# Optimization experiments

Measured on AMD Instinct MI355X. Metric: run time of the kernel, lower is better.

## Reference

```python
import jax, jax.numpy as jnp
import numpy as np


def _encode(tab, idx):
    # tab: [F, V, D]; idx: [..., F] int -> sum_f tab[f, idx[..., f]] -> [..., D]
    g = jax.vmap(lambda t, i: t[i], in_axes=(0, -1), out_axes=0)(tab, idx)
    return g.sum(0)


def _diffuse(fea, ei, w, order):
    # fea: [N, D]; ei: [2, E]; w: [E] learned edge weights
    N = fea.shape[0]
    r, c = ei[0], ei[1]
    adj = jnp.zeros((N, N), fea.dtype).at[r, c].set(w).at[c, r].set(w)
    adj = adj + jnp.eye(N, dtype=fea.dtype)
    r_col_inv = adj.sum(1) ** -0.5  # from degree over axis 1
    r_row_inv = adj.sum(0) ** -0.5  # from degree over axis 0
    A = r_row_inv[:, None] * adj * r_col_inv[None, :]
    x = fea
    y = fea
    for _ in range(order):
        x = jax.lax.stop_gradient(A @ x)
        y = y + x
    return jax.lax.stop_gradient(y / (order + 1.0))


def setup_inputs():
    B, N, E, EMB, L, FA, FB, V = 512, 128, 512, 300, 5, 9, 3, 64
    k = jax.random.split(jax.random.key(0), 12)
    s = 0.02
    return {
        "order": 3,
        "x_atom": jax.random.randint(k[0], (B, N, FA), 0, V),
        "edge_index": jax.random.randint(k[1], (B, 2, E), 0, N),
        "edge_attr": jax.random.randint(k[2], (B, E, FB), 0, V),
        "atom_tab": jax.random.normal(k[3], (FA, V, EMB)) * s,
        "bond_tab_root": jax.random.normal(k[4], (FB, V, EMB)) * s,
        "edge_lin_w": jax.random.normal(k[5], (EMB,)) * s,
        "edge_lin_b": jnp.zeros(()),
        "bond_tabs": jax.random.normal(k[6], (L, FB, V, EMB)) * s,
        "eps": jnp.zeros((L,)),
        "w1": jax.random.normal(k[7], (L, EMB, 2 * EMB)) * s,
        "b1": jnp.zeros((L, 2 * EMB)),
        "bn1_g": jnp.ones((L, 2 * EMB)),
        "bn1_b": jnp.zeros((L, 2 * EMB)),
        "w2": jax.random.normal(k[8], (L, 2 * EMB, EMB)) * s,
        "b2": jnp.zeros((L, EMB)),
        "bn_g": jnp.ones((L, EMB)),
        "bn_b": jnp.zeros((L, EMB)),
    }


def reference(order, x_atom, edge_index, edge_attr, atom_tab, bond_tab_root,
              edge_lin_w, edge_lin_b, bond_tabs, eps, w1, b1, bn1_g, bn1_b,
              w2, b2, bn_g, bn_b):
    B, N = x_atom.shape[:2]
    E = edge_index.shape[-1]
    L = w1.shape[0]
    DROP = 0.2  # node-feature drop rate (eval-mode scaling)

    # --- per-graph dense-adjacency diffusion (vmapped over graphs) ---
    fea = _encode(atom_tab, x_atom) * (1.0 - DROP)                 # [B, N, D]
    e_emb = _encode(bond_tab_root, edge_attr)                      # [B, E, D]
    ew = jax.nn.sigmoid(e_emb @ edge_lin_w + edge_lin_b)           # [B, E]
    h = jax.vmap(_diffuse, in_axes=(0, 0, 0, None))(fea, edge_index, ew, order)
    h = h.reshape(B * N, -1)                                       # [B*N, D]

    # --- globally-batched GIN message passing ---
    off = (jnp.arange(B) * N)[:, None]
    src = (edge_index[:, 0, :] + off).reshape(-1)                  # [B*E]
    dst = (edge_index[:, 1, :] + off).reshape(-1)
    ea_flat = edge_attr.reshape(B * E, -1)

    for l in range(L):
        ee = _encode(bond_tabs[l], ea_flat)                        # [B*E, D]
        msg = jax.nn.relu(h[src] + ee)
        agg = jax.ops.segment_sum(msg, dst, num_segments=B * N)
        z = (1.0 + eps[l]) * h + agg
        z = z @ w1[l] + b1[l]
        z = bn1_g[l] * z + bn1_b[l]   # eval-mode BN (running mean 0, var 1)
        z = jax.nn.relu(z)
        z = z @ w2[l] + b2[l]
        z = bn_g[l] * z + bn_b[l]     # outer eval-mode BN
        if l < L - 1:
            z = jax.nn.relu(z)
        h = z
    return h
```

## Files before the change

### kernel.cpp

```cpp
#include <hip/hip_runtime.h>

#define NGRAPH 512
#define NNODE  128
#define NEDGE  512
#define EMB    300
#define NLAYER 5
#define FA     9
#define FB     3
#define VV     64
#define KPAD   136

typedef __bf16 bf16x8 __attribute__((ext_vector_type(8)));
typedef __bf16 bf16x4 __attribute__((ext_vector_type(4)));
typedef float  f32x4  __attribute__((ext_vector_type(4)));

__device__ __forceinline__ void gload_lds16(const void* gptr, void* lptr) {
    __builtin_amdgcn_global_load_lds(
        (const __attribute__((address_space(1))) void*)gptr,
        (__attribute__((address_space(3))) void*)lptr, 16, 0, 0);
}

__global__ __launch_bounds__(256)
void prep_w_kernel(const float* __restrict__ w1, const float* __restrict__ w2,
                   __bf16* __restrict__ w1t, __bf16* __restrict__ w2t)
{
    const int i = blockIdx.x * 256 + threadIdx.x;
    const int T1 = NLAYER * 640 * 320;
    const int T2 = NLAYER * 320 * 640;
    if (i < T1) {
        const int l = i / (640 * 320);
        const int r = i - l * 640 * 320;
        const int n = r / 320, k = r - n * 320;
        float v = (n < 600 && k < 300) ? w1[((size_t)l * 300 + k) * 600 + n] : 0.f;
        w1t[i] = (__bf16)v;
    } else if (i < T1 + T2) {
        const int j = i - T1;
        const int l = j / (320 * 640);
        const int r = j - l * 320 * 640;
        const int n = r / 640, k = r - n * 640;
        float v = (n < 300 && k < 600) ? w2[((size_t)l * 600 + k) * 300 + n] : 0.f;
        w2t[j] = (__bf16)v;
    }
}

__global__ __launch_bounds__(512)
void adj_kernel(const int* __restrict__ edge_index,
                const int* __restrict__ edge_attr,
                const float* __restrict__ bond_tab_root,
                const float* __restrict__ edge_lin_w,
                const float* __restrict__ edge_lin_b,
                __bf16* __restrict__ Ahi_g, __bf16* __restrict__ Alo_g)
{
    __shared__ float A[128 * 129];
    __shared__ float ew_s[NEDGE];
    __shared__ int   es[NEDGE];
    __shared__ float rinv[128];
    __shared__ float cinv[128];

    const int tid = threadIdx.x;
    const int g   = blockIdx.x;
    int* Ai = (int*)A;

    for (int e = tid; e < NEDGE; e += 512) {
        int r = edge_index[(g * 2 + 0) * NEDGE + e];
        int c = edge_index[(g * 2 + 1) * NEDGE + e];
        es[e] = r | (c << 8);
    }
    for (int i = tid; i < 128 * 129; i += 512) Ai[i] = -1;
    __syncthreads();

    {
        const int wave = tid >> 6, lane = tid & 63;
        const float elb = edge_lin_b[0];
        for (int e = wave * 64; e < wave * 64 + 64; ++e) {
            const int base = (g * NEDGE + e) * 3;
            const int a0 = edge_attr[base + 0];
            const int a1 = edge_attr[base + 1];
            const int a2 = edge_attr[base + 2];
            const float* t0 = bond_tab_root + (0 * VV + a0) * EMB;
            const float* t1 = bond_tab_root + (1 * VV + a1) * EMB;
            const float* t2 = bond_tab_root + (2 * VV + a2) * EMB;
            float acc = 0.f;
            for (int d = lane; d < EMB; d += 64)
                acc += (t0[d] + t1[d] + t2[d]) * edge_lin_w[d];
            #pragma unroll
            for (int off = 32; off > 0; off >>= 1) acc += __shfl_xor(acc, off, 64);
            if (lane == 0) ew_s[e] = 1.f / (1.f + expf(-(acc + elb)));
        }
    }
    for (int e = tid; e < NEDGE; e += 512) {
        int r = es[e] & 255, c = es[e] >> 8;
        atomicMax(&Ai[r * 129 + c], e);
        atomicMax(&Ai[c * 129 + r], 512 + e);
    }
    __syncthreads();
    for (int i = tid; i < 128 * 129; i += 512) {
        int p = Ai[i];
        A[i] = (p < 0) ? 0.f : ew_s[p & 511];
    }
    __syncthreads();
    if (tid < 128) A[tid * 129 + tid] += 1.f;
    __syncthreads();
    if (tid < 128) {
        float rs = 0.f, cs = 0.f;
        for (int j = 0; j < 128; ++j) { rs += A[tid * 129 + j]; cs += A[j * 129 + tid]; }
        rinv[tid] = 1.f / sqrtf(rs);
        cinv[tid] = 1.f / sqrtf(cs);
    }
    __syncthreads();
    for (int i = tid; i < 128 * KPAD; i += 512) {
        const int m = i / KPAD, k = i - m * KPAD;
        float v = (k < 128) ? A[m * 129 + k] * cinv[m] * rinv[k] : 0.f;
        __bf16 hi = (__bf16)v;
        Ahi_g[(size_t)g * 128 * KPAD + i] = hi;
        Alo_g[(size_t)g * 128 * KPAD + i] = (__bf16)(v - (float)hi);
    }
}

__global__ __launch_bounds__(512)
void diffuse_mm_kernel(const int* __restrict__ order_p,
                       const int* __restrict__ x_atom,
                       const float* __restrict__ atom_tab,
                       const __bf16* __restrict__ Ahi_g,
                       const __bf16* __restrict__ Alo_g,
                       float* __restrict__ h)
{
    __shared__ __bf16 Ahi[128 * KPAD];
    __shared__ __bf16 Alo[128 * KPAD];
    __shared__ __bf16 xt[4 * 64 * KPAD];
    __shared__ int    xat[128 * FA];

    const int tid  = threadIdx.x;
    const int g    = blockIdx.x;
    const int lane = tid & 63;
    const int wid  = tid >> 6;
    const int wm   = (wid >> 1) * 32;
    const int wn   = (wid & 1) * 32;
    const int lr   = lane & 15;
    const int q4   = (lane >> 4) * 4;
    const int kc   = (lane >> 4) * 8;

    for (int idx = tid; idx < 128 * KPAD / 8; idx += 512) {
        gload_lds16(Ahi_g + (size_t)g * 128 * KPAD + idx * 8, (char*)Ahi + idx * 16);
        gload_lds16(Alo_g + (size_t)g * 128 * KPAD + idx * 8, (char*)Alo + idx * 16);
    }
    for (int i = tid; i < 128 * FA; i += 512) xat[i] = x_atom[g * 128 * FA + i];
    __syncthreads();

    const int   ord    = order_p[0];
    const float yscale = 1.f / (float)(ord + 1);

    for (int cb = 0; cb < 5; ++cb) {
        const int dbase = cb * 64;

        float yacc[2][2][4];
        #pragma unroll
        for (int mi = 0; mi < 2; ++mi) {
            #pragma unroll
            for (int ni = 0; ni < 2; ++ni) {
                const int n_ = wn + ni * 16 + lr;
                const int d  = dbase + n_;
                #pragma unroll
                for (int r = 0; r < 4; ++r) {
                    const int m_ = wm + mi * 16 + q4 + r;
                    float v = 0.f;
                    if (d < EMB) {
                        #pragma unroll
                        for (int f = 0; f < FA; ++f)
                            v += atom_tab[(size_t)((f << 6) + xat[m_ * FA + f]) * EMB + d];
                        v *= 0.8f;
                    }
                    yacc[mi][ni][r] = v;
                    __bf16 hi = (__bf16)v;
                    xt[0 * 64 * KPAD + n_ * KPAD + m_] = hi;
                    xt[1 * 64 * KPAD + n_ * KPAD + m_] = (__bf16)(v - (float)hi);
                }
            }
        }
        __syncthreads();

        int curbuf = 0;
        for (int o = 0; o < ord; ++o) {
            const __bf16* xh = xt + (curbuf * 2 + 0) * 64 * KPAD;
            const __bf16* xl = xt + (curbuf * 2 + 1) * 64 * KPAD;
            f32x4 racc[2][2];
            #pragma unroll
            for (int mi = 0; mi < 2; ++mi)
                #pragma unroll
                for (int ni = 0; ni < 2; ++ni) racc[mi][ni] = (f32x4){0.f, 0.f, 0.f, 0.f};

            #pragma unroll
            for (int ks = 0; ks < 4; ++ks) {
                const int k0 = ks * 32 + kc;
                bf16x8 ah[2], al[2], bh[2], bl[2];
                #pragma unroll
                for (int mi = 0; mi < 2; ++mi) {
                    ah[mi] = *(const bf16x8*)&Ahi[(wm + mi * 16 + lr) * KPAD + k0];
                    al[mi] = *(const bf16x8*)&Alo[(wm + mi * 16 + lr) * KPAD + k0];
                }
                #pragma unroll
                for (int ni = 0; ni < 2; ++ni) {
                    bh[ni] = *(const bf16x8*)&xh[(wn + ni * 16 + lr) * KPAD + k0];
                    bl[ni] = *(const bf16x8*)&xl[(wn + ni * 16 + lr) * KPAD + k0];
                }
                #pragma unroll
                for (int mi = 0; mi < 2; ++mi) {
                    #pragma unroll
                    for (int ni = 0; ni < 2; ++ni) {
                        racc[mi][ni] = __builtin_amdgcn_mfma_f32_16x16x32_bf16(
                            ah[mi], bh[ni], racc[mi][ni], 0, 0, 0);
                        racc[mi][ni] = __builtin_amdgcn_mfma_f32_16x16x32_bf16(
                            ah[mi], bl[ni], racc[mi][ni], 0, 0, 0);
                        racc[mi][ni] = __builtin_amdgcn_mfma_f32_16x16x32_bf16(
                            al[mi], bh[ni], racc[mi][ni], 0, 0, 0);
                    }
                }
            }

            __bf16* nh = xt + ((curbuf ^ 1) * 2 + 0) * 64 * KPAD;
            __bf16* nl = xt + ((curbuf ^ 1) * 2 + 1) * 64 * KPAD;
            #pragma unroll
            for (int mi = 0; mi < 2; ++mi) {
                #pragma unroll
                for (int ni = 0; ni < 2; ++ni) {
                    const int n_ = wn + ni * 16 + lr;
                    const int mbase = wm + mi * 16 + q4;
                    bf16x4 hv, lv;
                    #pragma unroll
                    for (int r = 0; r < 4; ++r) {
                        const float v = racc[mi][ni][r];
                        yacc[mi][ni][r] += v;
                        __bf16 hi = (__bf16)v;
                        hv[r] = hi;
                        lv[r] = (__bf16)(v - (float)hi);
                    }
                    *(bf16x4*)&nh[n_ * KPAD + mbase] = hv;
                    *(bf16x4*)&nl[n_ * KPAD + mbase] = lv;
                }
            }
            __syncthreads();
            curbuf ^= 1;
        }

        #pragma unroll
        for (int mi = 0; mi < 2; ++mi) {
            #pragma unroll
            for (int ni = 0; ni < 2; ++ni) {
                const int n_ = wn + ni * 16 + lr;
                const int d  = dbase + n_;
                if (d < EMB) {
                    #pragma unroll
                    for (int r = 0; r < 4; ++r) {
                        const int m_ = wm + mi * 16 + q4 + r;
                        h[(size_t)(g * 128 + m_) * EMB + d] = yacc[mi][ni][r] * yscale;
                    }
                }
            }
        }
    }
}

__global__ __launch_bounds__(1024)
void agg_kernel(const int* __restrict__ edge_index,
                const int* __restrict__ edge_attr,
                const float* __restrict__ bond_tabs,
                const float* __restrict__ eps_all,
                const int l,
                const float* __restrict__ h,
                __bf16* __restrict__ zb)
{
    __shared__ __bf16         hs[128 * 160];
    __shared__ int            epk[NEDGE];
    __shared__ unsigned short eord[NEDGE];
    __shared__ int            cnt[128];
    __shared__ int            off_[129];
    __shared__ int            fill[128];

    const int tid  = threadIdx.x;
    const int g    = blockIdx.x >> 1;
    const int coff = (blockIdx.x & 1) * 160;
    const int wave = tid >> 6, lane = tid & 63;
    const float epl = 1.f + eps_all[l];
    const float* bt = bond_tabs + (size_t)l * FB * VV * EMB;

    if (tid < 128) { cnt[tid] = 0; fill[tid] = 0; }
    __syncthreads();
    if (tid < NEDGE) {
        const int s_ = edge_index[(g * 2 + 0) * NEDGE + tid];
        const int d_ = edge_index[(g * 2 + 1) * NEDGE + tid];
        const int base = (g * NEDGE + tid) * 3;
        epk[tid] = s_ | (d_ << 7) | (edge_attr[base + 0] << 14)
                 | (edge_attr[base + 1] << 20) | (edge_attr[base + 2] << 26);
        atomicAdd(&cnt[d_], 1);
    }
    for (int idx = tid; idx < 128 * 40; idx += 1024) {
        const int r = idx / 40, q = (idx - r * 40) * 4;
        bf16x4 v;
        #pragma unroll
        for (int j = 0; j < 4; ++j) {
            const int d = coff + q + j;
            v[j] = (__bf16)((d < EMB) ? h[(size_t)(g * 128 + r) * EMB + d] : 0.f);
        }
        *(bf16x4*)&hs[r * 160 + q] = v;
    }
    __syncthreads();
    if (tid < 64) {
        const int a = cnt[tid];
        const int b = cnt[64 + tid];
        int ia = a;
        #pragma unroll
        for (int o = 1; o < 64; o <<= 1) {
            int t = __shfl_up(ia, o, 64);
            if (tid >= o) ia += t;
        }
        const int totA = __shfl(ia, 63, 64);
        int ib = b;
        #pragma unroll
        for (int o = 1; o < 64; o <<= 1) {
            int t = __shfl_up(ib, o, 64);
            if (tid >= o) ib += t;
        }
        off_[tid]      = ia - a;
        off_[64 + tid] = totA + ib - b;
        if (tid == 63) off_[128] = totA + ib;
    }
    __syncthreads();
    if (tid < NEDGE) {
        const int d_ = (epk[tid] >> 7) & 127;
        const int pos = off_[d_] + atomicAdd(&fill[d_], 1);
        eord[pos] = (unsigned short)tid;
    }
    __syncthreads();

    const int d0 = lane, d1 = lane + 64, d2 = lane + 128;
    const bool r0 = (coff + d0) < EMB;
    const bool r1 = (coff + d1) < EMB;
    const bool r2 = (d2 < 160) && ((coff + d2) < EMB);

    for (int n = wave; n < 128; n += 16) {
        const float* hrow = h + (size_t)(g * 128 + n) * EMB + coff;
        float a0 = r0 ? epl * hrow[d0] : 0.f;
        float a1 = r1 ? epl * hrow[d1] : 0.f;
        float a2 = r2 ? epl * hrow[d2] : 0.f;
        const int eEnd = off_[n + 1];
        for (int ee = off_[n]; ee < eEnd; ++ee) {
            const int p   = epk[eord[ee]];
            const int src = p & 127;
            const float* t0 = bt + ((p >> 14) & 63) * EMB + coff;
            const float* t1 = bt + (64  + ((p >> 20) & 63)) * EMB + coff;
            const float* t2 = bt + (128 + ((p >> 26) & 63)) * EMB + coff;
            if (r0) a0 += fmaxf((float)hs[src * 160 + d0] + t0[d0] + t1[d0] + t2[d0], 0.f);
            if (r1) a1 += fmaxf((float)hs[src * 160 + d1] + t0[d1] + t1[d1] + t2[d1], 0.f);
            if (r2) a2 += fmaxf((float)hs[src * 160 + d2] + t0[d2] + t1[d2] + t2[d2], 0.f);
        }
        __bf16* zrow = zb + (size_t)(g * 128 + n) * 320 + coff;
        zrow[d0] = (__bf16)a0;
        zrow[d1] = (__bf16)a1;
        if (d2 < 160) zrow[d2] = (__bf16)a2;
    }
}

template <int CBF16, int RELU>
__global__ __launch_bounds__(256)
void gemm_mfma(const __bf16* __restrict__ A, const int lda,
               const int nT, const int nBlkN, const __bf16* __restrict__ B,
               void* __restrict__ Cv, const int ldc, const int Nreal,
               const float* __restrict__ bias, const float* __restrict__ gam,
               const float* __restrict__ bet)
{
    __shared__ unsigned short As[256 * 32];
    __shared__ unsigned short Bs[64 * 32];

    const int tid  = threadIdx.x;
    const int nwg  = gridDim.x;
    const int hw   = blockIdx.x;
    const int lg   = (hw & 7) * (nwg >> 3) + (hw >> 3);
    const int bn   = (lg % nBlkN) * 64;
    const int bm   = (lg / nBlkN) * 256;
    const int wid  = tid >> 6;
    const int lane = tid & 63;
    const int wm   = wid * 64;
    const int lr   = lane & 15;
    const int kc   = (lane >> 4) * 8;
    const int q4   = (lane >> 4) * 4;
    const int KP   = nT * 32;

    f32x4 acc[4][4];
    #pragma unroll
    for (int mi = 0; mi < 4; ++mi)
        #pragma unroll
        for (int ni = 0; ni < 4; ++ni) acc[mi][ni] = (f32x4){0.f, 0.f, 0.f, 0.f};

    for (int t = 0; t < nT; ++t) {
        const int k0 = t * 32;
        {
            const int n = tid >> 2, k8 = (tid & 3) * 8;
            gload_lds16(B + (size_t)(bn + n) * KP + k0 + k8,
                        (char*)Bs + tid * 16);
        }
        #pragma unroll
        for (int q = 0; q < 4; ++q) {
            const int idx = q * 256 + tid;
            const int m = idx >> 2, k8 = (idx & 3) * 8;
            gload_lds16(A + (size_t)(bm + m) * lda + k0 + k8,
                        (char*)As + idx * 16);
        }
        __syncthreads();

        bf16x8 a[4], b[4];
        #pragma unroll
        for (int mi = 0; mi < 4; ++mi)
            a[mi] = *(const bf16x8*)&As[(wm + mi * 16 + lr) * 32 + kc];
        #pragma unroll
        for (int ni = 0; ni < 4; ++ni)
            b[ni] = *(const bf16x8*)&Bs[(ni * 16 + lr) * 32 + kc];
        #pragma unroll
        for (int mi = 0; mi < 4; ++mi)
            #pragma unroll
            for (int ni = 0; ni < 4; ++ni)
                acc[mi][ni] = __builtin_amdgcn_mfma_f32_16x16x32_bf16(
                    a[mi], b[ni], acc[mi][ni], 0, 0, 0);
        __syncthreads();
    }

    #pragma unroll
    for (int ni = 0; ni < 4; ++ni) {
        const int n = bn + ni * 16 + lr;
        const bool nv = (n < Nreal);
        const float gv = nv ? gam[n]  : 0.f;
        const float bv = nv ? bias[n] : 0.f;
        const float ev = nv ? bet[n]  : 0.f;
        #pragma unroll
        for (int mi = 0; mi < 4; ++mi) {
            #pragma unroll
            for (int r = 0; r < 4; ++r) {
                const size_t m = bm + wm + mi * 16 + q4 + r;
                float v = gv * (acc[mi][ni][r] + bv) + ev;
                if (RELU) v = fmaxf(v, 0.f);
                if (CBF16) {
                    ((__bf16*)Cv)[m * ldc + n] = (__bf16)v;
                } else if (nv) {
                    ((float*)Cv)[m * ldc + n] = v;
                }
            }
        }
    }
}

extern "C" void kernel_launch(void* const* d_in, const int* in_sizes, int n_in,
                              void* d_out, int out_size, void* d_ws, size_t ws_size,
                              hipStream_t stream)
{
    const int*   order_p       = (const int*)d_in[0];
    const int*   x_atom        = (const int*)d_in[1];
    const int*   edge_index    = (const int*)d_in[2];
    const int*   edge_attr     = (const int*)d_in[3];
    const float* atom_tab      = (const float*)d_in[4];
    const float* bond_tab_root = (const float*)d_in[5];
    const float* edge_lin_w    = (const float*)d_in[6];
    const float* edge_lin_b    = (const float*)d_in[7];
    const float* bond_tabs     = (const float*)d_in[8];
    const float* eps           = (const float*)d_in[9];
    const float* w1            = (const float*)d_in[10];
    const float* b1            = (const float*)d_in[11];
    const float* bn1g          = (const float*)d_in[12];
    const float* bn1b          = (const float*)d_in[13];
    const float* w2            = (const float*)d_in[14];
    const float* b2            = (const float*)d_in[15];
    const float* bng           = (const float*)d_in[16];
    const float* bnb           = (const float*)d_in[17];

    float* h = (float*)d_out;

    char* ws = (char*)d_ws;
    __bf16* Ahi_g = (__bf16*)ws;
    __bf16* Alo_g = (__bf16*)(ws + 17825792);
    __bf16* z1    = (__bf16*)ws;
    __bf16* w1t   = (__bf16*)(ws + 83886080);
    __bf16* w2t   = (__bf16*)(ws + 83886080 + 2048000);
    __bf16* zb    = (__bf16*)(ws + 83886080 + 4096000);

    prep_w_kernel<<<8000, 256, 0, stream>>>(w1, w2, w1t, w2t);

    adj_kernel<<<NGRAPH, 512, 0, stream>>>(edge_index, edge_attr, bond_tab_root,
                                           edge_lin_w, edge_lin_b, Ahi_g, Alo_g);

    diffuse_mm_kernel<<<NGRAPH, 512, 0, stream>>>(order_p, x_atom, atom_tab,
                                                  Ahi_g, Alo_g, h);

    for (int l = 0; l < NLAYER; ++l) {
        agg_kernel<<<NGRAPH * 2, 1024, 0, stream>>>(
            edge_index, edge_attr, bond_tabs, eps, l, h, zb);

        gemm_mfma<1, 1><<<2560, 256, 0, stream>>>(
            zb, 320, 10, 10, w1t + (size_t)l * 640 * 320,
            z1, 640, 600, b1 + l * 600, bn1g + l * 600, bn1b + l * 600);

        if (l < NLAYER - 1) {
            gemm_mfma<0, 1><<<1280, 256, 0, stream>>>(
                z1, 640, 20, 5, w2t + (size_t)l * 320 * 640,
                h, EMB, 300, b2 + l * 300, bng + l * 300, bnb + l * 300);
        } else {
            gemm_mfma<0, 0><<<1280, 256, 0, stream>>>(
                z1, 640, 20, 5, w2t + (size_t)l * 320 * 640,
                h, EMB, 300, b2 + l * 300, bng + l * 300, bnb + l * 300);
        }
    }
}
```

Measured before the change: 1.206 ms.

## Fuse the two MLP GEMMs into one kernel with the intermediate held in LDS

Replaces the two separate bf16 MFMA GEMM launches per layer with a single mlp_kernel. Each 32-row block stages its aggregated input in LDS, computes the 600-wide hidden activation into shared memory, then immediately runs the second GEMM. This removes the global round trip of the 65536x640 intermediate and one launch per layer. In exchange, weight tiles are read straight from global/L2 without LDS staging and are reused only across 32 rows, and w2t is padded to 384 rows.

```diff
diff --git a/kernel.cpp b/kernel.cpp
--- a/kernel.cpp
+++ b/kernel.cpp
@@ -26,7 +26,7 @@
 {
     const int i = blockIdx.x * 256 + threadIdx.x;
     const int T1 = NLAYER * 640 * 320;
-    const int T2 = NLAYER * 320 * 640;
+    const int T2 = NLAYER * 384 * 640;
     if (i < T1) {
         const int l = i / (640 * 320);
         const int r = i - l * 640 * 320;
@@ -35,8 +35,8 @@
         w1t[i] = (__bf16)v;
     } else if (i < T1 + T2) {
         const int j = i - T1;
-        const int l = j / (320 * 640);
-        const int r = j - l * 320 * 640;
+        const int l = j / (384 * 640);
+        const int r = j - l * 384 * 640;
         const int n = r / 640, k = r - n * 640;
         float v = (n < 300 && k < 600) ? w2[((size_t)l * 600 + k) * 300 + n] : 0.f;
         w2t[j] = (__bf16)v;
@@ -360,87 +360,121 @@
     }
 }
 
-template <int CBF16, int RELU>
-__global__ __launch_bounds__(256)
-void gemm_mfma(const __bf16* __restrict__ A, const int lda,
-               const int nT, const int nBlkN, const __bf16* __restrict__ B,
-               void* __restrict__ Cv, const int ldc, const int Nreal,
-               const float* __restrict__ bias, const float* __restrict__ gam,
-               const float* __restrict__ bet)
+template <int RELU>
+__global__ __launch_bounds__(512)
+void mlp_kernel(const __bf16* __restrict__ zb,
+                const __bf16* __restrict__ w1t_l,
+                const __bf16* __restrict__ w2t_l,
+                float* __restrict__ h,
+                const float* __restrict__ b1_l, const float* __restrict__ g1_l,
+                const float* __restrict__ e1_l,
+                const float* __restrict__ b2_l, const float* __restrict__ g2_l,
+                const float* __restrict__ e2_l)
 {
-    __shared__ unsigned short As[256 * 32];
-    __shared__ unsigned short Bs[64 * 32];
+    __shared__ __bf16 zbs[32 * 328];
+    __shared__ __bf16 zs[32 * 648];
 
     const int tid  = threadIdx.x;
-    const int nwg  = gridDim.x;
-    const int hw   = blockIdx.x;
-    const int lg   = (hw & 7) * (nwg >> 3) + (hw >> 3);
-    const int bn   = (lg % nBlkN) * 64;
-    const int bm   = (lg / nBlkN) * 256;
-    const int wid  = tid >> 6;
-    const int lane = tid & 63;
-    const int wm   = wid * 64;
+    const int bm   = blockIdx.x * 32;
+    const int wave = tid >> 6, lane = tid & 63;
     const int lr   = lane & 15;
     const int kc   = (lane >> 4) * 8;
     const int q4   = (lane >> 4) * 4;
-    const int KP   = nT * 32;
-
-    f32x4 acc[4][4];
-    #pragma unroll
-    for (int mi = 0; mi < 4; ++mi)
-        #pragma unroll
-        for (int ni = 0; ni < 4; ++ni) acc[mi][ni] = (f32x4){0.f, 0.f, 0.f, 0.f};
-
-    for (int t = 0; t < nT; ++t) {
-        const int k0 = t * 32;
-        {
-            const int n = tid >> 2, k8 = (tid & 3) * 8;
-            gload_lds16(B + (size_t)(bn + n) * KP + k0 + k8,
-                        (char*)Bs + tid * 16);
-        }
-        #pragma unroll
-        for (int q = 0; q < 4; ++q) {
-            const int idx = q * 256 + tid;
-            const int m = idx >> 2, k8 = (idx & 3) * 8;
-            gload_lds16(A + (size_t)(bm + m) * lda + k0 + k8,
-                        (char*)As + idx * 16);
-        }
-        __syncthreads();
-
-        bf16x8 a[4], b[4];
-        #pragma unroll
-        for (int mi = 0; mi < 4; ++mi)
-            a[mi] = *(const bf16x8*)&As[(wm + mi * 16 + lr) * 32 + kc];
-        #pragma unroll
-        for (int ni = 0; ni < 4; ++ni)
-            b[ni] = *(const bf16x8*)&Bs[(ni * 16 + lr) * 32 + kc];
-        #pragma unroll
-        for (int mi = 0; mi < 4; ++mi)
-            #pragma unroll
-            for (int ni = 0; ni < 4; ++ni)
-                acc[mi][ni] = __builtin_amdgcn_mfma_f32_16x16x32_bf16(
-                    a[mi], b[ni], acc[mi][ni], 0, 0, 0);
-        __syncthreads();
-    }
-
-    #pragma unroll
-    for (int ni = 0; ni < 4; ++ni) {
-        const int n = bn + ni * 16 + lr;
-        const bool nv = (n < Nreal);
-        const float gv = nv ? gam[n]  : 0.f;
-        const float bv = nv ? bias[n] : 0.f;
-        const float ev = nv ? bet[n]  : 0.f;
-        #pragma unroll
-        for (int mi = 0; mi < 4; ++mi) {
-            #pragma unroll
-            for (int r = 0; r < 4; ++r) {
-                const size_t m = bm + wm + mi * 16 + q4 + r;
-                float v = gv * (acc[mi][ni][r] + bv) + ev;
-                if (RELU) v = fmaxf(v, 0.f);
-                if (CBF16) {
-                    ((__bf16*)Cv)[m * ldc + n] = (__bf16)v;
-                } else if (nv) {
-                    ((float*)Cv)[m * ldc + n] = v;
+
+    for (int idx = tid; idx < 32 * 40; idx += 512) {
+        const int r = idx / 40, c = idx - r * 40;
+        bf16x8 v = *(const bf16x8*)&zb[(size_t)(bm + r) * 320 + c * 8];
+        *(bf16x8*)&zbs[r * 328 + c * 8] = v;
+    }
+    __syncthreads();
+
+    {
+        const int ncol0 = wave * 80;
+        f32x4 acc[2][5];
+        #pragma unroll
+        for (int mi = 0; mi < 2; ++mi)
+            #pragma unroll
+            for (int ni = 0; ni < 5; ++ni) acc[mi][ni] = (f32x4){0.f, 0.f, 0.f, 0.f};
+
+        #pragma unroll 2
+        for (int kt = 0; kt < 10; ++kt) {
+            const int k0 = kt * 32 + kc;
+            bf16x8 a[2], b[5];
+            #pragma unroll
+            for (int mi = 0; mi < 2; ++mi)
+                a[mi] = *(const bf16x8*)&zbs[(mi * 16 + lr) * 328 + k0];
+            #pragma unroll
+            for (int ni = 0; ni < 5; ++ni)
+                b[ni] = *(const bf16x8*)&w1t_l[(size_t)(ncol0 + ni * 16 + lr) * 320 + k0];
+            #pragma unroll
+            for (int mi = 0; mi < 2; ++mi)
+                #pragma unroll
+                for (int ni = 0; ni < 5; ++ni)
+                    acc[mi][ni] = __builtin_amdgcn_mfma_f32_16x16x32_bf16(
+                        a[mi], b[ni], acc[mi][ni], 0, 0, 0);
+        }
+        #pragma unroll
+        for (int ni = 0; ni < 5; ++ni) {
+            const int n = ncol0 + ni * 16 + lr;
+            const bool nv = (n < 600);
+            const float gv = nv ? g1_l[n] : 0.f;
+            const float bv = nv ? b1_l[n] : 0.f;
+            const float ev = nv ? e1_l[n] : 0.f;
+            #pragma unroll
+            for (int mi = 0; mi < 2; ++mi) {
+                #pragma unroll
+                for (int r = 0; r < 4; ++r) {
+                    const int m = mi * 16 + q4 + r;
+                    float v = gv * (acc[mi][ni][r] + bv) + ev;
+                    v = fmaxf(v, 0.f);
+                    zs[m * 648 + n] = (__bf16)v;
+                }
+            }
+        }
+    }
+    __syncthreads();
+
+    {
+        const int ncol0 = wave * 48;
+        f32x4 acc[2][3];
+        #pragma unroll
+        for (int mi = 0; mi < 2; ++mi)
+            #pragma unroll
+            for (int ni = 0; ni < 3; ++ni) acc[mi][ni] = (f32x4){0.f, 0.f, 0.f, 0.f};
+
+        #pragma unroll 2
+        for (int kt = 0; kt < 20; ++kt) {
+            const int k0 = kt * 32 + kc;
+            bf16x8 a[2], b[3];
+            #pragma unroll
+            for (int mi = 0; mi < 2; ++mi)
+                a[mi] = *(const bf16x8*)&zs[(mi * 16 + lr) * 648 + k0];
+            #pragma unroll
+            for (int ni = 0; ni < 3; ++ni)
+                b[ni] = *(const bf16x8*)&w2t_l[(size_t)(ncol0 + ni * 16 + lr) * 640 + k0];
+            #pragma unroll
+            for (int mi = 0; mi < 2; ++mi)
+                #pragma unroll
+                for (int ni = 0; ni < 3; ++ni)
+                    acc[mi][ni] = __builtin_amdgcn_mfma_f32_16x16x32_bf16(
+                        a[mi], b[ni], acc[mi][ni], 0, 0, 0);
+        }
+        #pragma unroll
+        for (int ni = 0; ni < 3; ++ni) {
+            const int n = ncol0 + ni * 16 + lr;
+            if (n < 300) {
+                const float gv = g2_l[n];
+                const float bv = b2_l[n];
+                const float ev = e2_l[n];
+                #pragma unroll
+                for (int mi = 0; mi < 2; ++mi) {
+                    #pragma unroll
+                    for (int r = 0; r < 4; ++r) {
+                        const int m = mi * 16 + q4 + r;
+                        float v = gv * (acc[mi][ni][r] + bv) + ev;
+                        if (RELU) v = fmaxf(v, 0.f);
+                        h[(size_t)(bm + m) * EMB + n] = v;
+                    }
                 }
             }
         }
@@ -475,12 +509,11 @@
     char* ws = (char*)d_ws;
     __bf16* Ahi_g = (__bf16*)ws;
     __bf16* Alo_g = (__bf16*)(ws + 17825792);
-    __bf16* z1    = (__bf16*)ws;
     __bf16* w1t   = (__bf16*)(ws + 83886080);
     __bf16* w2t   = (__bf16*)(ws + 83886080 + 2048000);
-    __bf16* zb    = (__bf16*)(ws + 83886080 + 4096000);
-
-    prep_w_kernel<<<8000, 256, 0, stream>>>(w1, w2, w1t, w2t);
+    __bf16* zb    = (__bf16*)(ws + 83886080 + 2048000 + 2457600);
+
+    prep_w_kernel<<<8800, 256, 0, stream>>>(w1, w2, w1t, w2t);
 
     adj_kernel<<<NGRAPH, 512, 0, stream>>>(edge_index, edge_attr, bond_tab_root,
                                            edge_lin_w, edge_lin_b, Ahi_g, Alo_g);
@@ -492,18 +525,16 @@
         agg_kernel<<<NGRAPH * 2, 1024, 0, stream>>>(
             edge_index, edge_attr, bond_tabs, eps, l, h, zb);
 
-        gemm_mfma<1, 1><<<2560, 256, 0, stream>>>(
-            zb, 320, 10, 10, w1t + (size_t)l * 640 * 320,
-            z1, 640, 600, b1 + l * 600, bn1g + l * 600, bn1b + l * 600);
-
         if (l < NLAYER - 1) {
-            gemm_mfma<0, 1><<<1280, 256, 0, stream>>>(
-                z1, 640, 20, 5, w2t + (size_t)l * 320 * 640,
-                h, EMB, 300, b2 + l * 300, bng + l * 300, bnb + l * 300);
+            mlp_kernel<1><<<2048, 512, 0, stream>>>(
+                zb, w1t + (size_t)l * 640 * 320, w2t + (size_t)l * 384 * 640, h,
+                b1 + l * 600, bn1g + l * 600, bn1b + l * 600,
+                b2 + l * 300, bng + l * 300, bnb + l * 300);
         } else {
-            gemm_mfma<0, 0><<<1280, 256, 0, stream>>>(
-                z1, 640, 20, 5, w2t + (size_t)l * 320 * 640,
-                h, EMB, 300, b2 + l * 300, bng + l * 300, bnb + l * 300);
-        }
-    }
-}
+            mlp_kernel<0><<<2048, 512, 0, stream>>>(
+                zb, w1t + (size_t)l * 640 * 320, w2t + (size_t)l * 384 * 640, h,
+                b1 + l * 600, bn1g + l * 600, bn1b + l * 600,
+                b2 + l * 300, bng + l * 300, bnb + l * 300);
+        }
+    }
+}
```

After: 1.683 ms. +39.5%, slower.
